# Optimization experiments

Measured on AMD Instinct MI355X. Metric: run time of the kernel, lower is better.

## Reference

```python
import jax, jax.numpy as jnp
import numpy as np

B, T_IN, T_OUT, N, FEAT = 32, 96, 96, 512, 8
HID = 512
GRID_SIZE, SPLINE_ORDER = 5, 3
GRID_RANGE = (-1.0, 1.0)


def _make_grid():
    # matches KANLinear.create_grid: identical row per in_feature, so keep 1-D
    h = (GRID_RANGE[1] - GRID_RANGE[0]) / GRID_SIZE
    return jnp.arange(-SPLINE_ORDER, GRID_SIZE + SPLINE_ORDER + 1, dtype=jnp.float32) * h + GRID_RANGE[0]


def _b_splines(x, grid):
    # x: [M, in_features]; de Boor-Cox recursion, order SPLINE_ORDER
    x = x[..., None]  # [M, in, 1]
    bases = ((x >= grid[:-1]) & (x < grid[1:])).astype(x.dtype)
    for k in range(1, SPLINE_ORDER + 1):
        left = (x - grid[:-(k + 1)]) / (grid[k:-1] - grid[:-(k + 1)])
        right = (grid[k + 1:] - x) / (grid[k + 1:] - grid[1:-k])
        bases = left * bases[..., :-1] + right * bases[..., 1:]
    return bases  # [M, in, grid_size + spline_order]


def setup_inputs() -> dict:
    key = jax.random.key(0)
    ks = jax.random.split(key, 12)
    s = 0.05
    return {
        "X": jax.random.normal(ks[0], (B, T_IN, N, FEAT), jnp.float32),
        "Y": jax.random.normal(ks[1], (B, T_OUT, N, FEAT), jnp.float32),
        "Wx": jax.random.normal(ks[2], (HID, T_IN * FEAT), jnp.float32) * s,
        "bx": jax.random.normal(ks[3], (HID,), jnp.float32) * s,
        "Wy": jax.random.normal(ks[4], (HID, T_OUT * FEAT), jnp.float32) * s,
        "by": jax.random.normal(ks[5], (HID,), jnp.float32) * s,
        "base_w": jax.random.normal(ks[6], (64, 2 * HID), jnp.float32) * s,
        "spline_w": jax.random.normal(ks[7], (64, 2 * HID, GRID_SIZE + SPLINE_ORDER), jnp.float32) * s,
        "spline_scaler": jax.random.normal(ks[8], (64, 2 * HID), jnp.float32) * s,
        "Wf": jax.random.normal(ks[9], (T_OUT * FEAT, 64), jnp.float32) * s,
        "bf": jax.random.normal(ks[10], (T_OUT * FEAT,), jnp.float32) * s,
    }


def reference(X, Y, Wx, bx, Wy, by, base_w, spline_w, spline_scaler, Wf, bf):
    # [B, T, N, F] -> [B, N, T*F]
    Xf = jnp.transpose(X, (0, 2, 1, 3)).reshape(B, N, T_IN * FEAT)
    Yf = jnp.transpose(Y, (0, 2, 1, 3)).reshape(B, N, T_OUT * FEAT)
    Hx = jnp.tanh(Xf @ Wx.T + bx)
    Hy = jnp.tanh(Yf @ Wy.T + by)
    h = jnp.concatenate([Hx, Hy], axis=-1).reshape(B * N, 2 * HID)

    grid = _make_grid()
    base_out = jax.nn.silu(h) @ base_w.T
    scaled_sw = spline_w * spline_scaler[..., None]  # [out, in, coeff]
    spline_out = jnp.einsum("mik,oik->mo", _b_splines(h, grid), scaled_sw)
    kan_out = (base_out + spline_out).reshape(B, N, 64)

    out = kan_out @ Wf.T + bf  # [B, N, T_OUT*FEAT]
    out = out.reshape(B, N, T_OUT, FEAT)
    return jnp.transpose(out, (0, 2, 1, 3))  # [B, T_OUT, N, FEAT]
```

## Files before the change

### kernel.cpp

```cpp
#include <hip/hip_runtime.h>
#include <cmath>

#define B_    32
#define T_    96
#define N_    512
#define F_    8
#define TF_   768
#define HID_  512
#define M_    16384
#define KIN_  1024
#define KS_   8

typedef short short8 __attribute__((ext_vector_type(8)));
typedef float f32x4  __attribute__((ext_vector_type(4)));
typedef unsigned int  uintx4 __attribute__((ext_vector_type(4)));
typedef unsigned long long ulongx2 __attribute__((ext_vector_type(2)));
typedef _Float16 halfx8 __attribute__((ext_vector_type(8)));
typedef unsigned short      ushort_t;
typedef unsigned int        uint_t;
typedef unsigned long long  ulong_t;

#define HT_B     0ull
#define WQ_B     33554432ull
#define WB_B     34734080ull
#define SH_B     36306944ull
#define KANR_B   61472768ull
#define WFQ_B    63569920ull

static __device__ inline uint_t  fbits(float f){ return __builtin_bit_cast(uint_t, f); }
static __device__ inline ushort_t f2b(float f){
    uint_t u = fbits(f);
    return (ushort_t)((u + 0x7fffu + ((u >> 16) & 1u)) >> 16);
}
static __device__ inline float b2f(ushort_t h){ return __builtin_bit_cast(float, (uint_t)h << 16); }
static __device__ inline ulong_t pack4(float4 v){
    return (ulong_t)f2b(v.x) | ((ulong_t)f2b(v.y) << 16) |
           ((ulong_t)f2b(v.z) << 32) | ((ulong_t)f2b(v.w) << 48);
}
static __device__ inline ulong_t pack4t(float4 v){
    uint_t d0 = (fbits(v.x) >> 16) | (fbits(v.y) & 0xffff0000u);
    uint_t d1 = (fbits(v.z) >> 16) | (fbits(v.w) & 0xffff0000u);
    return (ulong_t)d0 | ((ulong_t)d1 << 32);
}
static __device__ inline float fast_tanh(float x){
    const float e = __expf(2.0f * x);
    return 1.0f - 2.0f / (e + 1.0f);
}
static __device__ inline void gload_lds16(const void* g, void* l){
    __builtin_amdgcn_global_load_lds(
        (const __attribute__((address_space(1))) unsigned int*)g,
        (__attribute__((address_space(3))) unsigned int*)l, 16, 0, 0);
}

__global__ __launch_bounds__(256) void pack_wq(
    const float* __restrict__ base_w,
    const float* __restrict__ spline_w,
    const float* __restrict__ scaler,
    ushort_t* __restrict__ wq)
{
    const int e = blockIdx.x * 256 + threadIdx.x;
    const int j    = e & 7;
    const int ln   = (e >> 3) & 63;
    const int ct   = (e >> 9) & 3;
    const int t    = (e >> 11) & 3;
    const int rest = e >> 13;
    const int ss   = rest % 9;
    const int ks   = rest / 9;
    const int o = ct * 16 + (ln & 15);
    const int g = ln >> 4;
    float v;
    if (ss < 8) {
        const int i = ks * 128 + ss * 16 + t * 4 + g;
        v = spline_w[(o * KIN_ + i) * 8 + j] * scaler[o * KIN_ + i];
    } else {
        const int i = ks * 128 + t * 32 + g * 8 + j;
        v = base_w[o * KIN_ + i];
    }
    wq[e] = f2b(v);
}

__global__ __launch_bounds__(256) void pack_wb2(
    const float* __restrict__ Wx,
    const float* __restrict__ Wy,
    ushort_t* __restrict__ wb)
{
    const int e = blockIdx.x * 256 + threadIdx.x;
    const float v = (e < 512 * TF_) ? Wx[e] : Wy[e - 512 * TF_];
    wb[e] = f2b(v);
}

__global__ __launch_bounds__(256) void pack_wfq(
    const float* __restrict__ Wf, ushort_t* __restrict__ wfq)
{
    const int e = blockIdx.x * 256 + threadIdx.x;
    const int jj  = e & 7;
    const int ln  = (e >> 3) & 63;
    const int rt  = (e >> 9) & 3;
    const int s   = (e >> 11) & 1;
    const int wvt = (e >> 12) & 1;
    const int tb  = e >> 13;
    const int tf = tb * 128 + wvt * 64 + rt * 16 + (ln & 15);
    const int o  = s * 32 + (ln >> 4) * 8 + jj;
    wfq[e] = f2b(Wf[(size_t)tf * 64 + o]);
}

__global__ __launch_bounds__(256) void xcvt_kernel(
    const float* __restrict__ Xs, ushort_t* __restrict__ xbf)
{
    __shared__ __align__(16) char lds[32 * 1552];
    const int tid = threadIdx.x;
    const int n0  = blockIdx.x * 32;
    const int bb  = blockIdx.y;
    const int nl  = (tid & 63) >> 1;
    const int f4  = (tid & 1) * 4;
    const int tq  = tid >> 6;
    #pragma unroll 4
    for (int u = 0; u < 24; u++) {
        const int t = u * 4 + tq;
        const float4 v = *(const float4*)(Xs + (size_t)bb * (T_ * N_ * F_)
                                             + (size_t)t * (N_ * F_)
                                             + (size_t)(n0 + nl) * F_ + f4);
        *(ulong_t*)(lds + nl * 1552 + t * 16 + f4 * 2) = pack4t(v);
    }
    __syncthreads();
    #pragma unroll 4
    for (int u = 0; u < 12; u++) {
        const int c   = u * 256 + tid;
        const int row = c / 96;
        const int col = c - row * 96;
        const uintx4 val = *(const uintx4*)(lds + row * 1552 + col * 16);
        *(uintx4*)(xbf + (size_t)(bb * 512 + n0 + row) * TF_ + col * 8) = val;
    }
}

__global__ __launch_bounds__(512, 2) void gemm_tanh_v7(
    const ushort_t* __restrict__ xbf,
    const ushort_t* __restrict__ wb,
    const float* __restrict__ bias,
    ushort_t* __restrict__ ht, int z)
{
    __shared__ __align__(16) char smem[32768];

    const int tid = threadIdx.x;
    const int wv  = tid >> 6;
    const int ln  = tid & 63;
    const int lr  = ln & 15;
    const int hi  = ln >> 4;
    const int wm  = wv >> 2;
    const int wj  = wv & 3;

    const int m0  = blockIdx.x * 128;
    const int jl0 = blockIdx.y * 128;
    const int j0  = z * 512 + jl0;

    const int r_l = ln >> 3;
    const int ck  = ((ln & 7) ^ r_l) * 8;

    f32x4 acc[4][2] = {};

    for (int kt = 0; kt < 12; kt++) {
        __syncthreads();
        #pragma unroll
        for (int s = 0; s < 2; s++) {
            const int reg = s * 8 + wv;
            const int row = reg * 8 + r_l;
            gload_lds16(xbf + (size_t)(m0 + row) * TF_ + kt * 64 + ck,
                        smem + reg * 1024 + ln * 16);
            gload_lds16(wb + (size_t)(j0 + row) * TF_ + kt * 64 + ck,
                        smem + 16384 + reg * 1024 + ln * 16);
        }
        __syncthreads();

        #pragma unroll
        for (int h = 0; h < 2; h++) {
            const int g = h * 4 + hi;
            short8 a[4], b[2];
            #pragma unroll
            for (int rt = 0; rt < 4; rt++) {
                const int r = wm * 64 + rt * 16 + lr;
                a[rt] = *(short8*)(smem + r * 128 + ((g ^ (r & 7)) * 16));
            }
            #pragma unroll
            for (int ct = 0; ct < 2; ct++) {
                const int r = wj * 32 + ct * 16 + lr;
                b[ct] = *(short8*)(smem + 16384 + r * 128 + ((g ^ (r & 7)) * 16));
            }
            #pragma unroll
            for (int rt = 0; rt < 4; rt++)
                #pragma unroll
                for (int ct = 0; ct < 2; ct++)
                    acc[rt][ct] = __builtin_amdgcn_mfma_f32_16x16x32_bf16(
                        a[rt], b[ct], acc[rt][ct], 0, 0, 0);
        }
    }

    __syncthreads();
    #pragma unroll
    for (int ct = 0; ct < 2; ct++) {
        const int j = wj * 32 + ct * 16 + lr;
        const float bvv = bias[jl0 + j];
        #pragma unroll
        for (int rt = 0; rt < 4; rt++) {
            const f32x4 v = acc[rt][ct];
            float4 tv;
            tv.x = fast_tanh(v[0] + bvv);
            tv.y = fast_tanh(v[1] + bvv);
            tv.z = fast_tanh(v[2] + bvv);
            tv.w = fast_tanh(v[3] + bvv);
            const int slot = wm * 8 + rt * 2 + (hi >> 1);
            *(ulong_t*)(smem + j * 256 + ((slot ^ (j & 15)) * 16) + (hi & 1) * 8)
                = pack4(tv);
        }
    }
    __syncthreads();
    {
        const int j  = tid >> 2;
        const int q4 = tid & 3;
        ushort_t* dst = ht + (size_t)(j0 + j) * M_ + m0 + q4 * 32;
        #pragma unroll
        for (int w = 0; w < 4; w++) {
            const int slot = q4 * 4 + w;
            short8 val = *(short8*)(smem + j * 256 + ((slot ^ (j & 15)) * 16));
            *(short8*)(dst + w * 8) = val;
        }
    }
}

static __device__ inline short8 eval_bases(float x)
{
    const float v = fmaf(x, 2.5f, 2.5f);
    float sf = floorf(v);
    sf = fminf(fmaxf(sf, 0.0f), 4.0f);
    const float u = v - sf;
    const int si = (int)sf;
    const float u2 = u * u, u3 = u2 * u;
    const float omu = 1.0f - u;
    const float omu3 = omu * omu * omu;
    const float Bb0 = omu3 * (1.0f / 6.0f);
    const float Bb3 = u3 * (1.0f / 6.0f);
    const float Bb1 = fmaf(0.5f, u3, 2.0f / 3.0f) - u2;
    const float Bb2 = 1.0f - Bb0 - Bb1 - Bb3;
    const uint_t d0 = (fbits(Bb0) >> 16) | (fbits(Bb1) & 0xffff0000u);
    const uint_t d1 = (fbits(Bb2) >> 16) | (fbits(Bb3) & 0xffff0000u);
    const ulong_t P = (ulong_t)d0 | ((ulong_t)d1 << 32);
    const int sh = si << 4;
    const ulong_t Plo = P << (sh & 63);
    const ulong_t Phi = P >> ((64 - sh) & 63);
    ulongx2 pr;
    pr.x = (si == 4) ? 0ull : Plo;
    pr.y = (si == 0) ? 0ull : ((si == 4) ? P : Phi);
    return __builtin_bit_cast(short8, pr);
}

__global__ __launch_bounds__(256) void kan_v5(
    const ushort_t* __restrict__ ht,
    const ushort_t* __restrict__ wq,
    _Float16* __restrict__ kanp)
{
    const int tid = threadIdx.x;
    const int wv  = tid >> 6;
    const int ln  = tid & 63;
    const int g   = ln >> 4;
    const int lr  = ln & 15;
    const int m0  = blockIdx.x * 64;
    const int ks  = blockIdx.y;
    const int iB  = ks * 128;
    const size_t r0 = (size_t)(m0 + wv * 16 + lr);

    const short8* wqf = (const short8*)wq + (size_t)ks * 9216 + ln;
    const ushort_t* htg  = ht + (size_t)(iB + g) * M_ + r0;
    const ushort_t* htg8 = ht + (size_t)(iB + g * 8) * M_ + r0;

    f32x4 acc[4] = {};

    for (int ss = 0; ss < 8; ss++) {
        #pragma unroll
        for (int t = 0; t < 4; t++) {
            const short8* bp = wqf + (size_t)(ss * 4 + t) * 256;
            const short8 b0 = bp[0], b1 = bp[64], b2 = bp[128], b3 = bp[192];
            const short8 a0 = eval_bases(b2f(htg[(size_t)(ss * 16 + t * 4) * M_]));
            acc[0] = __builtin_amdgcn_mfma_f32_16x16x32_bf16(a0, b0, acc[0], 0, 0, 0);
            acc[1] = __builtin_amdgcn_mfma_f32_16x16x32_bf16(a0, b1, acc[1], 0, 0, 0);
            acc[2] = __builtin_amdgcn_mfma_f32_16x16x32_bf16(a0, b2, acc[2], 0, 0, 0);
            acc[3] = __builtin_amdgcn_mfma_f32_16x16x32_bf16(a0, b3, acc[3], 0, 0, 0);
        }
    }
    #pragma unroll
    for (int t = 0; t < 4; t++) {
        const short8* bp = wqf + (size_t)(32 + t) * 256;
        const short8 b0 = bp[0], b1 = bp[64], b2 = bp[128], b3 = bp[192];
        uintx4 d;
        #pragma unroll
        for (int jj = 0; jj < 4; jj++) {
            const float x0 = b2f(htg8[(size_t)(t * 32 + 2 * jj)     * M_]);
            const float x1 = b2f(htg8[(size_t)(t * 32 + 2 * jj + 1) * M_]);
            const float s0 = x0 / (1.0f + __expf(-x0));
            const float s1 = x1 / (1.0f + __expf(-x1));
            d[jj] = (fbits(s0) >> 16) | (fbits(s1) & 0xffff0000u);
        }
        const short8 a0 = __builtin_bit_cast(short8, d);
        acc[0] = __builtin_amdgcn_mfma_f32_16x16x32_bf16(a0, b0, acc[0], 0, 0, 0);
        acc[1] = __builtin_amdgcn_mfma_f32_16x16x32_bf16(a0, b1, acc[1], 0, 0, 0);
        acc[2] = __builtin_amdgcn_mfma_f32_16x16x32_bf16(a0, b2, acc[2], 0, 0, 0);
        acc[3] = __builtin_amdgcn_mfma_f32_16x16x32_bf16(a0, b3, acc[3], 0, 0, 0);
    }

    #pragma unroll
    for (int ct = 0; ct < 4; ct++) {
        const int o = ct * 16 + lr;
        #pragma unroll
        for (int q = 0; q < 4; q++) {
            const size_t row = (size_t)(m0 + wv * 16 + g * 4 + q);
            kanp[(size_t)ks * (M_ * 64) + row * 64 + o] = (_Float16)acc[ct][q];
        }
    }
}

__global__ __launch_bounds__(256) void reduce_kan(
    const _Float16* __restrict__ kanp, ushort_t* __restrict__ kanr)
{
    const int e8 = blockIdx.x * 256 + threadIdx.x;
    const size_t base = (size_t)e8 * 8;
    float s[8] = {};
    #pragma unroll
    for (int p = 0; p < KS_; p++) {
        const halfx8 v = *(const halfx8*)(kanp + (size_t)p * (M_ * 64) + base);
        #pragma unroll
        for (int j = 0; j < 8; j++) s[j] += (float)v[j];
    }
    float4 s0 = make_float4(s[0], s[1], s[2], s[3]);
    float4 s1 = make_float4(s[4], s[5], s[6], s[7]);
    ulongx2 outv;
    outv.x = pack4(s0);
    outv.y = pack4(s1);
    *(ulongx2*)(kanr + base) = outv;
}

__global__ __launch_bounds__(256) void final_v2(
    const ushort_t* __restrict__ kanr,
    const ushort_t* __restrict__ wfq,
    const float* __restrict__ bf,
    float* __restrict__ out)
{
    const int tid = threadIdx.x;
    const int wv  = tid >> 6;
    const int ln  = tid & 63;
    const int lr  = ln & 15;
    const int hi  = ln >> 4;
    const int wvm = wv >> 1;
    const int wvt = wv & 1;
    const int mb  = blockIdx.x;
    const int tb  = blockIdx.y;

    f32x4 acc[4][4] = {};

    #pragma unroll
    for (int s = 0; s < 2; s++) {
        short8 afr[4], bfr[4];
        #pragma unroll
        for (int rt = 0; rt < 4; rt++) {
            const size_t idx = ((size_t)(((tb * 2 + wvt) * 2 + s) * 4 + rt)) * 64 + ln;
            afr[rt] = ((const short8*)wfq)[idx];
        }
        #pragma unroll
        for (int ct = 0; ct < 4; ct++) {
            const int m = mb * 128 + wvm * 64 + ct * 16 + lr;
            bfr[ct] = *(const short8*)(kanr + (size_t)m * 64 + s * 32 + hi * 8);
        }
        #pragma unroll
        for (int rt = 0; rt < 4; rt++)
            #pragma unroll
            for (int ct = 0; ct < 4; ct++)
                acc[rt][ct] = __builtin_amdgcn_mfma_f32_16x16x32_bf16(
                    afr[rt], bfr[ct], acc[rt][ct], 0, 0, 0);
    }

    #pragma unroll
    for (int rt = 0; rt < 4; rt++) {
        const int tf0 = tb * 128 + wvt * 64 + rt * 16 + hi * 4;
        const float4 b4 = *(const float4*)&bf[tf0];
        const int t  = tf0 >> 3;
        const int f0 = tf0 & 7;
        #pragma unroll
        for (int ct = 0; ct < 4; ct++) {
            const int m = mb * 128 + wvm * 64 + ct * 16 + lr;
            const int bb = m >> 9;
            const int n  = m & 511;
            const f32x4 v = acc[rt][ct];
            float4 o4 = make_float4(v[0] + b4.x, v[1] + b4.y, v[2] + b4.z, v[3] + b4.w);
            *(float4*)&out[(size_t)bb * (T_ * N_ * F_)
                           + (size_t)t * (N_ * F_)
                           + (size_t)n * F_ + f0] = o4;
        }
    }
}

extern "C" void kernel_launch(void* const* d_in, const int* in_sizes, int n_in,
                              void* d_out, int out_size, void* d_ws, size_t ws_size,
                              hipStream_t stream)
{
    const float* X      = (const float*)d_in[0];
    const float* Y      = (const float*)d_in[1];
    const float* Wx     = (const float*)d_in[2];
    const float* bx     = (const float*)d_in[3];
    const float* Wy     = (const float*)d_in[4];
    const float* by     = (const float*)d_in[5];
    const float* base_w = (const float*)d_in[6];
    const float* spline_w = (const float*)d_in[7];
    const float* spline_scaler = (const float*)d_in[8];
    const float* Wf     = (const float*)d_in[9];
    const float* bf     = (const float*)d_in[10];

    float* out = (float*)d_out;
    ushort_t* ht   = (ushort_t*)((char*)d_ws + HT_B);
    ushort_t* wq   = (ushort_t*)((char*)d_ws + WQ_B);
    ushort_t* wb   = (ushort_t*)((char*)d_ws + WB_B);
    ushort_t* xbf  = (ushort_t*)((char*)d_ws + SH_B);
    _Float16* kanp = (_Float16*)((char*)d_ws + SH_B);
    ushort_t* kanr = (ushort_t*)((char*)d_ws + KANR_B);
    ushort_t* wfq  = (ushort_t*)((char*)d_ws + WFQ_B);

    pack_wq<<<2304, 256, 0, stream>>>(base_w, spline_w, spline_scaler, wq);
    pack_wb2<<<3072, 256, 0, stream>>>(Wx, Wy, wb);
    pack_wfq<<<192, 256, 0, stream>>>(Wf, wfq);

    xcvt_kernel<<<dim3(16, 32), 256, 0, stream>>>(X, xbf);
    gemm_tanh_v7<<<dim3(128, 4), 512, 0, stream>>>(xbf, wb, bx, ht, 0);
    xcvt_kernel<<<dim3(16, 32), 256, 0, stream>>>(Y, xbf);
    gemm_tanh_v7<<<dim3(128, 4), 512, 0, stream>>>(xbf, wb, by, ht, 1);

    kan_v5<<<dim3(M_ / 64, KS_), 256, 0, stream>>>(ht, wq, kanp);
    reduce_kan<<<512, 256, 0, stream>>>(kanp, kanr);
    final_v2<<<dim3(128, 6), 256, 0, stream>>>(kanr, wfq, bf, out);
}
```

Baseline: 144.6 us.

## Fuse split-K reduction into final GEMM, retile tanh GEMM, prefetch in KAN

Removes the reduce_kan kernel by summing the eight fp16 split-K partials inside the final GEMM, which now uses fp16 MFMA with an fp16-packed Wf. The tanh GEMM moves from 512 to 256 threads per block, with each wave computing a 4x4 tile instead of 4x2. The KAN kernel software-prefetches the next weights and inputs and raises wave priority around the MFMAs. The fused reduction rereads the partials once for each of the six output column blocks and sums them in fp16, which adds redundant memory traffic and some precision risk.

```diff
diff --git a/kernel.cpp b/kernel.cpp
--- a/kernel.cpp
+++ b/kernel.cpp
@@ -12,10 +12,10 @@
 #define KS_   8
 
 typedef short short8 __attribute__((ext_vector_type(8)));
+typedef _Float16 half8 __attribute__((ext_vector_type(8)));
 typedef float f32x4  __attribute__((ext_vector_type(4)));
 typedef unsigned int  uintx4 __attribute__((ext_vector_type(4)));
 typedef unsigned long long ulongx2 __attribute__((ext_vector_type(2)));
-typedef _Float16 halfx8 __attribute__((ext_vector_type(8)));
 typedef unsigned short      ushort_t;
 typedef unsigned int        uint_t;
 typedef unsigned long long  ulong_t;
@@ -24,7 +24,6 @@
 #define WQ_B     33554432ull
 #define WB_B     34734080ull
 #define SH_B     36306944ull
-#define KANR_B   61472768ull
 #define WFQ_B    63569920ull
 
 static __device__ inline uint_t  fbits(float f){ return __builtin_bit_cast(uint_t, f); }
@@ -89,8 +88,8 @@
     wb[e] = f2b(v);
 }
 
-__global__ __launch_bounds__(256) void pack_wfq(
-    const float* __restrict__ Wf, ushort_t* __restrict__ wfq)
+__global__ __launch_bounds__(256) void pack_wfq16(
+    const float* __restrict__ Wf, _Float16* __restrict__ wfq)
 {
     const int e = blockIdx.x * 256 + threadIdx.x;
     const int jj  = e & 7;
@@ -101,7 +100,7 @@
     const int tb  = e >> 13;
     const int tf = tb * 128 + wvt * 64 + rt * 16 + (ln & 15);
     const int o  = s * 32 + (ln >> 4) * 8 + jj;
-    wfq[e] = f2b(Wf[(size_t)tf * 64 + o]);
+    wfq[e] = (_Float16)Wf[(size_t)tf * 64 + o];
 }
 
 __global__ __launch_bounds__(256) void xcvt_kernel(
@@ -133,7 +132,7 @@
     }
 }
 
-__global__ __launch_bounds__(512, 2) void gemm_tanh_v7(
+__global__ __launch_bounds__(256) void gemm_tanh_v8(
     const ushort_t* __restrict__ xbf,
     const ushort_t* __restrict__ wb,
     const float* __restrict__ bias,
@@ -146,49 +145,49 @@
     const int ln  = tid & 63;
     const int lr  = ln & 15;
     const int hi  = ln >> 4;
-    const int wm  = wv >> 2;
-    const int wj  = wv & 3;
+    const int wm  = wv >> 1;
+    const int wj  = wv & 1;
 
     const int m0  = blockIdx.x * 128;
     const int jl0 = blockIdx.y * 128;
     const int j0  = z * 512 + jl0;
 
-    const int r_l = ln >> 3;
-    const int ck  = ((ln & 7) ^ r_l) * 8;
-
-    f32x4 acc[4][2] = {};
+    const int srow8 = tid >> 3;
+    const int sch   = tid & 7;
+
+    f32x4 acc[4][4] = {};
 
     for (int kt = 0; kt < 12; kt++) {
         __syncthreads();
         #pragma unroll
-        for (int s = 0; s < 2; s++) {
-            const int reg = s * 8 + wv;
-            const int row = reg * 8 + r_l;
+        for (int s = 0; s < 4; s++) {
+            const int row = s * 32 + srow8;
+            const int ck = (sch ^ (row & 7)) * 8;
             gload_lds16(xbf + (size_t)(m0 + row) * TF_ + kt * 64 + ck,
-                        smem + reg * 1024 + ln * 16);
+                        smem + row * 128 + sch * 16);
             gload_lds16(wb + (size_t)(j0 + row) * TF_ + kt * 64 + ck,
-                        smem + 16384 + reg * 1024 + ln * 16);
+                        smem + 16384 + row * 128 + sch * 16);
         }
         __syncthreads();
 
         #pragma unroll
         for (int h = 0; h < 2; h++) {
             const int g = h * 4 + hi;
-            short8 a[4], b[2];
+            short8 a[4], b[4];
             #pragma unroll
             for (int rt = 0; rt < 4; rt++) {
                 const int r = wm * 64 + rt * 16 + lr;
                 a[rt] = *(short8*)(smem + r * 128 + ((g ^ (r & 7)) * 16));
             }
             #pragma unroll
-            for (int ct = 0; ct < 2; ct++) {
-                const int r = wj * 32 + ct * 16 + lr;
+            for (int ct = 0; ct < 4; ct++) {
+                const int r = wj * 64 + ct * 16 + lr;
                 b[ct] = *(short8*)(smem + 16384 + r * 128 + ((g ^ (r & 7)) * 16));
             }
             #pragma unroll
             for (int rt = 0; rt < 4; rt++)
                 #pragma unroll
-                for (int ct = 0; ct < 2; ct++)
+                for (int ct = 0; ct < 4; ct++)
                     acc[rt][ct] = __builtin_amdgcn_mfma_f32_16x16x32_bf16(
                         a[rt], b[ct], acc[rt][ct], 0, 0, 0);
         }
@@ -196,8 +195,8 @@
 
     __syncthreads();
     #pragma unroll
-    for (int ct = 0; ct < 2; ct++) {
-        const int j = wj * 32 + ct * 16 + lr;
+    for (int ct = 0; ct < 4; ct++) {
+        const int j = wj * 64 + ct * 16 + lr;
         const float bvv = bias[jl0 + j];
         #pragma unroll
         for (int rt = 0; rt < 4; rt++) {
@@ -214,12 +213,12 @@
     }
     __syncthreads();
     {
-        const int j  = tid >> 2;
-        const int q4 = tid & 3;
-        ushort_t* dst = ht + (size_t)(j0 + j) * M_ + m0 + q4 * 32;
-        #pragma unroll
-        for (int w = 0; w < 4; w++) {
-            const int slot = q4 * 4 + w;
+        const int j    = tid >> 1;
+        const int half = tid & 1;
+        ushort_t* dst = ht + (size_t)(j0 + j) * M_ + m0 + half * 64;
+        #pragma unroll
+        for (int w = 0; w < 8; w++) {
+            const int slot = half * 8 + w;
             short8 val = *(short8*)(smem + j * 256 + ((slot ^ (j & 15)) * 16));
             *(short8*)(dst + w * 8) = val;
         }
@@ -252,7 +251,7 @@
     return __builtin_bit_cast(short8, pr);
 }
 
-__global__ __launch_bounds__(256) void kan_v5(
+__global__ __launch_bounds__(256) void kan_v6(
     const ushort_t* __restrict__ ht,
     const ushort_t* __restrict__ wq,
     _Float16* __restrict__ kanp)
@@ -273,22 +272,34 @@
 
     f32x4 acc[4] = {};
 
-    for (int ss = 0; ss < 8; ss++) {
-        #pragma unroll
-        for (int t = 0; t < 4; t++) {
-            const short8* bp = wqf + (size_t)(ss * 4 + t) * 256;
-            const short8 b0 = bp[0], b1 = bp[64], b2 = bp[128], b3 = bp[192];
-            const short8 a0 = eval_bases(b2f(htg[(size_t)(ss * 16 + t * 4) * M_]));
-            acc[0] = __builtin_amdgcn_mfma_f32_16x16x32_bf16(a0, b0, acc[0], 0, 0, 0);
-            acc[1] = __builtin_amdgcn_mfma_f32_16x16x32_bf16(a0, b1, acc[1], 0, 0, 0);
-            acc[2] = __builtin_amdgcn_mfma_f32_16x16x32_bf16(a0, b2, acc[2], 0, 0, 0);
-            acc[3] = __builtin_amdgcn_mfma_f32_16x16x32_bf16(a0, b3, acc[3], 0, 0, 0);
-        }
-    }
-    #pragma unroll
-    for (int t = 0; t < 4; t++) {
-        const short8* bp = wqf + (size_t)(32 + t) * 256;
-        const short8 b0 = bp[0], b1 = bp[64], b2 = bp[128], b3 = bp[192];
+    short8 nb0 = wqf[0], nb1 = wqf[64], nb2 = wqf[128], nb3 = wqf[192];
+    float  nx  = b2f(htg[0]);
+
+    #pragma unroll
+    for (int it = 0; it < 32; ++it) {
+        const short8 b0 = nb0, b1 = nb1, b2 = nb2, b3 = nb3;
+        const float  x  = nx;
+        const short8* bp = wqf + (size_t)(it + 1) * 256;
+        nb0 = bp[0]; nb1 = bp[64]; nb2 = bp[128]; nb3 = bp[192];
+        if (it < 31) {
+            const int nit = it + 1;
+            nx = b2f(htg[(size_t)((nit >> 2) * 16 + (nit & 3) * 4) * M_]);
+        }
+        const short8 a0 = eval_bases(x);
+        __builtin_amdgcn_s_setprio(1);
+        acc[0] = __builtin_amdgcn_mfma_f32_16x16x32_bf16(a0, b0, acc[0], 0, 0, 0);
+        acc[1] = __builtin_amdgcn_mfma_f32_16x16x32_bf16(a0, b1, acc[1], 0, 0, 0);
+        acc[2] = __builtin_amdgcn_mfma_f32_16x16x32_bf16(a0, b2, acc[2], 0, 0, 0);
+        acc[3] = __builtin_amdgcn_mfma_f32_16x16x32_bf16(a0, b3, acc[3], 0, 0, 0);
+        __builtin_amdgcn_s_setprio(0);
+    }
+    #pragma unroll
+    for (int t = 0; t < 4; ++t) {
+        const short8 b0 = nb0, b1 = nb1, b2 = nb2, b3 = nb3;
+        if (t < 3) {
+            const short8* bp = wqf + (size_t)(33 + t) * 256;
+            nb0 = bp[0]; nb1 = bp[64]; nb2 = bp[128]; nb3 = bp[192];
+        }
         uintx4 d;
         #pragma unroll
         for (int jj = 0; jj < 4; jj++) {
@@ -299,10 +310,12 @@
             d[jj] = (fbits(s0) >> 16) | (fbits(s1) & 0xffff0000u);
         }
         const short8 a0 = __builtin_bit_cast(short8, d);
+        __builtin_amdgcn_s_setprio(1);
         acc[0] = __builtin_amdgcn_mfma_f32_16x16x32_bf16(a0, b0, acc[0], 0, 0, 0);
         acc[1] = __builtin_amdgcn_mfma_f32_16x16x32_bf16(a0, b1, acc[1], 0, 0, 0);
         acc[2] = __builtin_amdgcn_mfma_f32_16x16x32_bf16(a0, b2, acc[2], 0, 0, 0);
         acc[3] = __builtin_amdgcn_mfma_f32_16x16x32_bf16(a0, b3, acc[3], 0, 0, 0);
+        __builtin_amdgcn_s_setprio(0);
     }
 
     #pragma unroll
@@ -316,29 +329,9 @@
     }
 }
 
-__global__ __launch_bounds__(256) void reduce_kan(
-    const _Float16* __restrict__ kanp, ushort_t* __restrict__ kanr)
-{
-    const int e8 = blockIdx.x * 256 + threadIdx.x;
-    const size_t base = (size_t)e8 * 8;
-    float s[8] = {};
-    #pragma unroll
-    for (int p = 0; p < KS_; p++) {
-        const halfx8 v = *(const halfx8*)(kanp + (size_t)p * (M_ * 64) + base);
-        #pragma unroll
-        for (int j = 0; j < 8; j++) s[j] += (float)v[j];
-    }
-    float4 s0 = make_float4(s[0], s[1], s[2], s[3]);
-    float4 s1 = make_float4(s[4], s[5], s[6], s[7]);
-    ulongx2 outv;
-    outv.x = pack4(s0);
-    outv.y = pack4(s1);
-    *(ulongx2*)(kanr + base) = outv;
-}
-
-__global__ __launch_bounds__(256) void final_v2(
-    const ushort_t* __restrict__ kanr,
-    const ushort_t* __restrict__ wfq,
+__global__ __launch_bounds__(256) void final_v3(
+    const _Float16* __restrict__ kanp,
+    const _Float16* __restrict__ wfq,
     const float* __restrict__ bf,
     float* __restrict__ out)
 {
@@ -356,22 +349,27 @@
 
     #pragma unroll
     for (int s = 0; s < 2; s++) {
-        short8 afr[4], bfr[4];
+        half8 afr[4], bfr[4];
         #pragma unroll
         for (int rt = 0; rt < 4; rt++) {
             const size_t idx = ((size_t)(((tb * 2 + wvt) * 2 + s) * 4 + rt)) * 64 + ln;
-            afr[rt] = ((const short8*)wfq)[idx];
+            afr[rt] = ((const half8*)wfq)[idx];
         }
         #pragma unroll
         for (int ct = 0; ct < 4; ct++) {
             const int m = mb * 128 + wvm * 64 + ct * 16 + lr;
-            bfr[ct] = *(const short8*)(kanr + (size_t)m * 64 + s * 32 + hi * 8);
+            const _Float16* bp = kanp + (size_t)m * 64 + s * 32 + hi * 8;
+            half8 sum = *(const half8*)bp;
+            #pragma unroll
+            for (int p = 1; p < KS_; p++)
+                sum += *(const half8*)(bp + (size_t)p * (M_ * 64));
+            bfr[ct] = sum;
         }
         #pragma unroll
         for (int rt = 0; rt < 4; rt++)
             #pragma unroll
             for (int ct = 0; ct < 4; ct++)
-                acc[rt][ct] = __builtin_amdgcn_mfma_f32_16x16x32_bf16(
+                acc[rt][ct] = __builtin_amdgcn_mfma_f32_16x16x32_f16(
                     afr[rt], bfr[ct], acc[rt][ct], 0, 0, 0);
     }
 
@@ -417,19 +415,17 @@
     ushort_t* wb   = (ushort_t*)((char*)d_ws + WB_B);
     ushort_t* xbf  = (ushort_t*)((char*)d_ws + SH_B);
     _Float16* kanp = (_Float16*)((char*)d_ws + SH_B);
-    ushort_t* kanr = (ushort_t*)((char*)d_ws + KANR_B);
-    ushort_t* wfq  = (ushort_t*)((char*)d_ws + WFQ_B);
+    _Float16* wfq  = (_Float16*)((char*)d_ws + WFQ_B);
 
     pack_wq<<<2304, 256, 0, stream>>>(base_w, spline_w, spline_scaler, wq);
     pack_wb2<<<3072, 256, 0, stream>>>(Wx, Wy, wb);
-    pack_wfq<<<192, 256, 0, stream>>>(Wf, wfq);
+    pack_wfq16<<<192, 256, 0, stream>>>(Wf, wfq);
 
     xcvt_kernel<<<dim3(16, 32), 256, 0, stream>>>(X, xbf);
-    gemm_tanh_v7<<<dim3(128, 4), 512, 0, stream>>>(xbf, wb, bx, ht, 0);
+    gemm_tanh_v8<<<dim3(128, 4), 256, 0, stream>>>(xbf, wb, bx, ht, 0);
     xcvt_kernel<<<dim3(16, 32), 256, 0, stream>>>(Y, xbf);
-    gemm_tanh_v7<<<dim3(128, 4), 512, 0, stream>>>(xbf, wb, by, ht, 1);
-
-    kan_v5<<<dim3(M_ / 64, KS_), 256, 0, stream>>>(ht, wq, kanp);
-    reduce_kan<<<512, 256, 0, stream>>>(kanp, kanr);
-    final_v2<<<dim3(128, 6), 256, 0, stream>>>(kanr, wfq, bf, out);
-}
+    gemm_tanh_v8<<<dim3(128, 4), 256, 0, stream>>>(xbf, wb, by, ht, 1);
+
+    kan_v6<<<dim3(M_ / 64, KS_), 256, 0, stream>>>(ht, wq, kanp);
+    final_v3<<<dim3(128, 6), 256, 0, stream>>>(kanp, wfq, bf, out);
+}
```

Result: slower. 162.6 us (+12.5%).
